# Performance work log

Measured on AMD Instinct MI355X. Metric: run time of the kernel, lower is better.

## Reference

```python
import jax, jax.numpy as jnp
import numpy as np

T = 8192        # tokens (batch*seq)
D = 1024        # d_model
H = 4096        # expert hidden = 4*d_model
E = 16          # num_expert
K = 2           # moe_top_k


def setup_inputs() -> dict:
    key = jax.random.key(0)
    ks = jax.random.split(key, 7)
    s_in = 1.0 / np.sqrt(D)
    s_h = 1.0 / np.sqrt(H)
    return {
        "moe_inp": jax.random.normal(ks[0], (T, D), dtype=jnp.float32),
        "Wg": jax.random.normal(ks[1], (D, E), dtype=jnp.float32) * s_in,
        "bg": jnp.zeros((E,), dtype=jnp.float32),
        "W1": jax.random.normal(ks[2], (E, D, H), dtype=jnp.float32) * s_in,
        "b1": jnp.zeros((E, H), dtype=jnp.float32),
        "W2": jax.random.normal(ks[3], (E, H, D), dtype=jnp.float32) * s_h,
        "b2": jnp.zeros((E, D), dtype=jnp.float32),
    }


def reference(moe_inp, Wg, bg, W1, b1, W2, b2):
    # --- NaiveGate: linear -> top-k -> softmax over selected logits ---
    logits = moe_inp @ Wg + bg                      # [T, E]
    topk_val, topk_idx = jax.lax.top_k(logits, K)   # [T, K]
    gate_score = jax.nn.softmax(topk_val, axis=-1)  # [T, K]

    # Per-(token, expert) combine weight: sum of gate scores of slots routed to e.
    # Equivalent to scatter(dispatch) -> expert MLP -> gather(combine) weighted sum.
    onehot = jax.nn.one_hot(topk_idx, E, dtype=moe_inp.dtype)  # [T, K, E]
    comb_w = jnp.einsum('tk,tke->te', gate_score, onehot)      # [T, E]

    out = jnp.zeros_like(moe_inp)
    for e in range(E):  # fixed small expert count
        h = jax.nn.relu(moe_inp @ W1[e] + b1[e])   # [T, H]
        y = h @ W2[e] + b2[e]                      # [T, D]
        out = out + comb_w[:, e:e + 1] * y
    return out
```

## Files before the change

### kernel.cpp

```cpp
#include <hip/hip_runtime.h>
#include <hip/hip_bf16.h>
#include <stdint.h>


#define Tn 8192
#define Dn 1024
#define Hn 4096
#define En 16

typedef __attribute__((ext_vector_type(8))) short bf16x8;
typedef __attribute__((ext_vector_type(4))) float f32x4;

__device__ __forceinline__ unsigned short f2bf(float f) {
    union { __hip_bfloat16 h; unsigned short u; } cv;
    cv.h = __float2bfloat16(f);
    return cv.u;
}
__device__ __forceinline__ float bf2f(unsigned short u) {
    union { unsigned int i; float f; } cv;
    cv.i = ((unsigned int)u) << 16;
    return cv.f;
}

__device__ __forceinline__ void gload_lds16(const void* gptr, void* lptr) {
    __builtin_amdgcn_global_load_lds(
        (const __attribute__((address_space(1))) uint32_t*)gptr,
        (__attribute__((address_space(3))) uint32_t*)lptr, 16, 0, 0);
}

__device__ __forceinline__ int swz_tile(int v, int total) {
    int q = total >> 3, r = total & 7;
    int x = v & 7, k = v >> 3;
    int b = (x < r) ? x * (q + 1) : r * (q + 1) + (x - r) * q;
    return b + k;
}

__device__ __forceinline__ int find_e(const int* __restrict__ mb, int gm) {
    int e = 0;
#pragma unroll
    for (int i = 1; i < En; i++) e += (mb[i] <= gm) ? 1 : 0;
    return e;
}

__device__ __forceinline__ void waitvm4()  { asm volatile("s_waitcnt vmcnt(4)" ::: "memory"); }
__device__ __forceinline__ void waitvm0()  { asm volatile("s_waitcnt vmcnt(0)" ::: "memory"); }
__device__ __forceinline__ void barrier_raw() { asm volatile("s_barrier" ::: "memory"); }

__device__ __forceinline__ bool better(float va, int ia, float vb, int ib) {
    return (va > vb) || (va == vb && ia < ib);
}

__global__ __launch_bounds__(256) void gate_kernel(
    const float* __restrict__ x, const float* __restrict__ Wg,
    const float* __restrict__ bg,
    int* cnt, int* tok_e, int* tok_pos, float* tok_w)
{
    __shared__ float wgt[16 * 1028];
    int tid = threadIdx.x;
    int t0 = blockIdx.x * 16;

#pragma unroll
    for (int i = 0; i < 64; i++) {
        int idx = i * 256 + tid;
        int k = idx >> 4, e = idx & 15;
        wgt[e * 1028 + k] = Wg[idx];
    }
    __syncthreads();

    int tok = tid >> 4, e = tid & 15;
    const float4* xr = reinterpret_cast<const float4*>(x + (size_t)(t0 + tok) * Dn);
    const float4* wr = reinterpret_cast<const float4*>(&wgt[e * 1028]);
    float acc = 0.f;
#pragma unroll 8
    for (int q = 0; q < 256; q++) {
        float4 xv = xr[q], wv = wr[q];
        acc += xv.x * wv.x + xv.y * wv.y + xv.z * wv.z + xv.w * wv.w;
    }
    acc += bg[e];

    float v0 = acc, v1 = -1e30f;
    int i0 = e, i1 = -1;
#pragma unroll
    for (int m = 1; m < 16; m <<= 1) {
        float ov0 = __shfl_xor(v0, m, 16); int oi0 = __shfl_xor(i0, m, 16);
        float ov1 = __shfl_xor(v1, m, 16); int oi1 = __shfl_xor(i1, m, 16);
        if (better(ov0, oi0, v0, i0)) {
            if (better(v0, i0, ov1, oi1)) { v1 = v0; i1 = i0; }
            else                          { v1 = ov1; i1 = oi1; }
            v0 = ov0; i0 = oi0;
        } else if (better(ov0, oi0, v1, i1)) {
            v1 = ov0; i1 = oi0;
        }
    }
    if (e == 0) {
        float ex = __expf(v1 - v0);
        float w0 = 1.f / (1.f + ex);
        float w1 = ex / (1.f + ex);
        int p0 = atomicAdd(&cnt[i0], 1);
        int p1 = atomicAdd(&cnt[i1], 1);
        int t = t0 + tok;
        tok_e[t * 2 + 0] = i0; tok_e[t * 2 + 1] = i1;
        tok_pos[t * 2 + 0] = p0; tok_pos[t * 2 + 1] = p1;
        tok_w[t * 2 + 0] = w0; tok_w[t * 2 + 1] = w1;
    }
}

__global__ void scan_kernel(const int* cnt, int* base, int* mb)
{
    if (threadIdx.x == 0 && blockIdx.x == 0) {
        int b = 0, m = 0;
        for (int e = 0; e < En; e++) {
            base[e] = b; mb[e] = m;
            b += cnt[e];
            m += (cnt[e] + 127) >> 7;
        }
        base[En] = b; mb[En] = m;
    }
}

__global__ __launch_bounds__(256) void gather_kernel(
    const float* __restrict__ x, const int* tok_e, const int* tok_pos,
    const int* base, unsigned short* xg)
{
    int t = blockIdx.x; int tid = threadIdx.x;
    int e0 = tok_e[2 * t], e1 = tok_e[2 * t + 1];
    int r0 = base[e0] + tok_pos[2 * t];
    int r1 = base[e1] + tok_pos[2 * t + 1];
    float4 v = *reinterpret_cast<const float4*>(x + (size_t)t * Dn + tid * 4);
    ushort4 u;
    u.x = f2bf(v.x); u.y = f2bf(v.y); u.z = f2bf(v.z); u.w = f2bf(v.w);
    *reinterpret_cast<ushort4*>(xg + (size_t)r0 * Dn + tid * 4) = u;
    *reinterpret_cast<ushort4*>(xg + (size_t)r1 * Dn + tid * 4) = u;
}

__global__ __launch_bounds__(512) void convT_kernel(
    const float* __restrict__ src, unsigned short* __restrict__ dst, int R, int C)
{
    int e = blockIdx.z;
    const float* s = src + (size_t)e * R * C;
    unsigned short* d = dst + (size_t)e * R * C;
    __shared__ float tile[64][65];
    int r0 = blockIdx.y * 64, c0 = blockIdx.x * 64;
    int tr = threadIdx.x >> 4;
    int tc4 = (threadIdx.x & 15) * 4;
    float4 v0 = *reinterpret_cast<const float4*>(s + (size_t)(r0 + tr) * C + c0 + tc4);
    float4 v1 = *reinterpret_cast<const float4*>(s + (size_t)(r0 + tr + 32) * C + c0 + tc4);
    tile[tr][tc4 + 0] = v0.x; tile[tr][tc4 + 1] = v0.y;
    tile[tr][tc4 + 2] = v0.z; tile[tr][tc4 + 3] = v0.w;
    tile[tr + 32][tc4 + 0] = v1.x; tile[tr + 32][tc4 + 1] = v1.y;
    tile[tr + 32][tc4 + 2] = v1.z; tile[tr + 32][tc4 + 3] = v1.w;
    __syncthreads();
    ushort4 u0, u1;
    u0.x = f2bf(tile[tc4 + 0][tr]);      u1.x = f2bf(tile[tc4 + 0][tr + 32]);
    u0.y = f2bf(tile[tc4 + 1][tr]);      u1.y = f2bf(tile[tc4 + 1][tr + 32]);
    u0.z = f2bf(tile[tc4 + 2][tr]);      u1.z = f2bf(tile[tc4 + 2][tr + 32]);
    u0.w = f2bf(tile[tc4 + 3][tr]);      u1.w = f2bf(tile[tc4 + 3][tr + 32]);
    *reinterpret_cast<ushort4*>(d + (size_t)(c0 + tr) * R + r0 + tc4) = u0;
    *reinterpret_cast<ushort4*>(d + (size_t)(c0 + tr + 32) * R + r0 + tc4) = u1;
}

template<bool G1>
__global__ __launch_bounds__(256, 3) void gemm128_kernel(
    const unsigned short* __restrict__ Ag, const unsigned short* __restrict__ Bg,
    const float* __restrict__ bias, unsigned short* __restrict__ outb,
    const int* __restrict__ cnt, const int* __restrict__ base,
    const int* __restrict__ mb)
{
    constexpr int KDIM = G1 ? Dn : Hn;
    constexpr int NOUT = G1 ? Hn : Dn;
    constexpr int NTN = NOUT / 128;
    constexpr int NT = KDIM / 32;
    __shared__ unsigned short ldsA[3][128 * 32];
    __shared__ unsigned short ldsB[3][128 * 32];

    int totalgm = mb[En];
    int total = totalgm * NTN;

    int tid = threadIdx.x;
    int lane = tid & 63;
    int w = tid >> 6;
    int wm = (w >> 1) * 64, wn = (w & 1) * 64;
    int lr16 = lane & 15, lk = lane >> 4;
    int lj = lk * 4;

    int r0t = tid >> 2;
    int r1t = (tid + 256) >> 2;
    int col0 = (tid & 3) ^ (r0t & 3);
    int col1 = (tid & 3) ^ (r1t & 3);

    int aoff[4], boff[4];
#pragma unroll
    for (int m = 0; m < 4; m++) {
        int row = wm + m * 16 + lr16;
        aoff[m] = row * 32 + ((lk ^ (row & 3)) << 3);
    }
#pragma unroll
    for (int n = 0; n < 4; n++) {
        int row = wn + n * 16 + lr16;
        boff[n] = row * 32 + ((lk ^ (row & 3)) << 3);
    }

    for (int v = blockIdx.x; v < total; v += gridDim.x) {
        int tile = swz_tile(v, total);
        int nt = tile / totalgm;
        int gm = tile - nt * totalgm;
        int e = find_e(mb, gm);
        int mtile = gm - mb[e];
        int M_e = cnt[e];
        int m0 = mtile * 128, n0 = nt * 128;
        int rowbase0 = base[e] + m0;
        const unsigned short* Ab = Ag + (size_t)rowbase0 * KDIM;
        const unsigned short* Bb = Bg + ((size_t)e * NOUT + n0) * KDIM;

        const unsigned short* aS0 = Ab + (size_t)r0t * KDIM + col0 * 8;
        const unsigned short* aS1 = Ab + (size_t)r1t * KDIM + col1 * 8;
        const unsigned short* bS0 = Bb + (size_t)r0t * KDIM + col0 * 8;
        const unsigned short* bS1 = Bb + (size_t)r1t * KDIM + col1 * 8;

        f32x4 acc[4][4];
#pragma unroll
        for (int m = 0; m < 4; m++)
#pragma unroll
            for (int n = 0; n < 4; n++) acc[m][n] = (f32x4){0.f, 0.f, 0.f, 0.f};

        auto stage = [&](int t, int sl) {
            char* sa = (char*)ldsA[sl];
            char* sb = (char*)ldsB[sl];
            int k0 = t * 32;
            gload_lds16(aS0 + k0, sa + tid * 16);
            gload_lds16(aS1 + k0, sa + (tid + 256) * 16);
            gload_lds16(bS0 + k0, sb + tid * 16);
            gload_lds16(bS1 + k0, sb + (tid + 256) * 16);
        };

        stage(0, 0);
        stage(1, 1);

        int cur = 0, nxt2 = 2;
        for (int t = 0; t < NT; ++t) {
            if (t + 1 < NT) waitvm4();
            else            waitvm0();
            barrier_raw();
            if (t + 2 < NT) stage(t + 2, nxt2);
            const unsigned short* sa = ldsA[cur];
            const unsigned short* sb = ldsB[cur];
            bf16x8 a[4], b[4];
#pragma unroll
            for (int n = 0; n < 4; n++) b[n] = *(const bf16x8*)(sb + boff[n]);
#pragma unroll
            for (int m = 0; m < 4; m++) a[m] = *(const bf16x8*)(sa + aoff[m]);
            __builtin_amdgcn_s_setprio(1);
#pragma unroll
            for (int m = 0; m < 4; m++)
#pragma unroll
                for (int n = 0; n < 4; n++)
                    acc[m][n] = __builtin_amdgcn_mfma_f32_16x16x32_bf16(b[n], a[m], acc[m][n], 0, 0, 0);
            __builtin_amdgcn_s_setprio(0);
            cur = (cur == 2) ? 0 : cur + 1;
            nxt2 = (nxt2 == 2) ? 0 : nxt2 + 1;
        }

        const float* be = bias + (size_t)e * NOUT;
#pragma unroll
        for (int m = 0; m < 4; m++) {
            int rt = wm + m * 16 + lr16;
            if (m0 + rt < M_e) {
                size_t rowoff = (size_t)(rowbase0 + rt) * NOUT;
#pragma unroll
                for (int n = 0; n < 4; n++) {
                    int col0e = n0 + wn + n * 16 + lj;
                    float4 bs = *reinterpret_cast<const float4*>(be + col0e);
                    float v0 = acc[m][n][0] + bs.x;
                    float v1 = acc[m][n][1] + bs.y;
                    float v2 = acc[m][n][2] + bs.z;
                    float v3 = acc[m][n][3] + bs.w;
                    ushort4 u;
                    if constexpr (G1) {
                        u.x = f2bf(fmaxf(v0, 0.f));
                        u.y = f2bf(fmaxf(v1, 0.f));
                        u.z = f2bf(fmaxf(v2, 0.f));
                        u.w = f2bf(fmaxf(v3, 0.f));
                    } else {
                        u.x = f2bf(v0); u.y = f2bf(v1);
                        u.z = f2bf(v2); u.w = f2bf(v3);
                    }
                    *reinterpret_cast<ushort4*>(outb + rowoff + col0e) = u;
                }
            }
        }
    }
}

__global__ __launch_bounds__(256) void combine_kernel(
    const unsigned short* __restrict__ y,
    const int* __restrict__ tok_e, const int* __restrict__ tok_pos,
    const int* __restrict__ base, const float* __restrict__ tok_w,
    float* __restrict__ out)
{
    int t = blockIdx.x, tid = threadIdx.x;
    int e0 = tok_e[2 * t], e1 = tok_e[2 * t + 1];
    int r0 = base[e0] + tok_pos[2 * t];
    int r1 = base[e1] + tok_pos[2 * t + 1];
    float w0 = tok_w[2 * t], w1 = tok_w[2 * t + 1];
    ushort4 a = *reinterpret_cast<const ushort4*>(y + (size_t)r0 * Dn + tid * 4);
    ushort4 b = *reinterpret_cast<const ushort4*>(y + (size_t)r1 * Dn + tid * 4);
    float4 o;
    o.x = w0 * bf2f(a.x) + w1 * bf2f(b.x);
    o.y = w0 * bf2f(a.y) + w1 * bf2f(b.y);
    o.z = w0 * bf2f(a.z) + w1 * bf2f(b.z);
    o.w = w0 * bf2f(a.w) + w1 * bf2f(b.w);
    *reinterpret_cast<float4*>(out + (size_t)t * Dn + tid * 4) = o;
}

extern "C" void kernel_launch(void* const* d_in, const int* in_sizes, int n_in,
                              void* d_out, int out_size, void* d_ws, size_t ws_size,
                              hipStream_t stream)
{
    const float* x  = (const float*)d_in[0];
    const float* Wg = (const float*)d_in[1];
    const float* bg = (const float*)d_in[2];
    const float* W1 = (const float*)d_in[3];
    const float* b1 = (const float*)d_in[4];
    const float* W2 = (const float*)d_in[5];
    const float* b2 = (const float*)d_in[6];
    float* out = (float*)d_out;

    char* ws = (char*)d_ws;
    size_t off = 0;
    auto alloc = [&](size_t bytes) {
        size_t o = off; off += (bytes + 255) & ~(size_t)255; return o;
    };
    const int ROWS = Tn * 2;
    const int RCAP = ROWS + 256;

    unsigned short* Wt = (unsigned short*)(ws + alloc((size_t)En * Hn * Dn * 2));
    unsigned short* xg = (unsigned short*)(ws + alloc((size_t)RCAP * Dn * 2));
    unsigned short* hg = (unsigned short*)(ws + alloc((size_t)RCAP * Hn * 2));
    unsigned short* yv = (unsigned short*)(ws + alloc((size_t)RCAP * Dn * 2));
    int*   cnt     = (int*)(ws + alloc(En * 4));
    int*   base    = (int*)(ws + alloc((En + 1) * 4));
    int*   mb      = (int*)(ws + alloc((En + 1) * 4));
    int*   tok_e   = (int*)(ws + alloc(Tn * 2 * 4));
    int*   tok_pos = (int*)(ws + alloc(Tn * 2 * 4));
    float* tok_w   = (float*)(ws + alloc(Tn * 2 * 4));
    (void)ws_size; (void)in_sizes; (void)n_in; (void)out_size;

    hipMemsetAsync(cnt, 0, En * 4, stream);

    gate_kernel<<<Tn / 16, 256, 0, stream>>>(x, Wg, bg, cnt, tok_e, tok_pos, tok_w);
    scan_kernel<<<1, 64, 0, stream>>>(cnt, base, mb);
    gather_kernel<<<Tn, 256, 0, stream>>>(x, tok_e, tok_pos, base, xg);

    convT_kernel<<<dim3(Hn / 64, Dn / 64, En), 512, 0, stream>>>(W1, Wt, Dn, Hn);
    gemm128_kernel<true><<<768, 256, 0, stream>>>(
        xg, Wt, b1, hg, cnt, base, mb);

    convT_kernel<<<dim3(Dn / 64, Hn / 64, En), 512, 0, stream>>>(W2, Wt, Hn, Dn);
    gemm128_kernel<false><<<768, 256, 0, stream>>>(
        hg, Wt, b2, yv, cnt, base, mb);

    combine_kernel<<<Tn, 256, 0, stream>>>(yv, tok_e, tok_pos, base, tok_w, out);
}
```

Baseline: 742.7 us.

## Switch expert GEMM to double-buffered LDS with 8-chunk swizzle and higher occupancy

Expert GEMM drops from triple to double buffering (48KB to 32KB of LDS per block), allowing 5 blocks per CU instead of 3, and the persistent grid grows from 768 to 1280 blocks. The LDS layout packs two 32-wide K rows into one 64-element line with an XOR swizzle over 8 chunks, aiming to reduce bank conflicts. The cost is a shallower prefetch: each iteration waits for all outstanding loads (vmcnt 0), so latency hiding has to come from more resident waves rather than a deeper pipeline. Register pressure under launch_bounds(256,5) may also force spills.

```diff
diff --git a/kernel.cpp b/kernel.cpp
--- a/kernel.cpp
+++ b/kernel.cpp
@@ -42,7 +42,6 @@
     return e;
 }
 
-__device__ __forceinline__ void waitvm4()  { asm volatile("s_waitcnt vmcnt(4)" ::: "memory"); }
 __device__ __forceinline__ void waitvm0()  { asm volatile("s_waitcnt vmcnt(0)" ::: "memory"); }
 __device__ __forceinline__ void barrier_raw() { asm volatile("s_barrier" ::: "memory"); }
 
@@ -160,7 +159,7 @@
 }
 
 template<bool G1>
-__global__ __launch_bounds__(256, 3) void gemm128_kernel(
+__global__ __launch_bounds__(256, 5) void gemm128_kernel(
     const unsigned short* __restrict__ Ag, const unsigned short* __restrict__ Bg,
     const float* __restrict__ bias, unsigned short* __restrict__ outb,
     const int* __restrict__ cnt, const int* __restrict__ base,
@@ -170,8 +169,8 @@
     constexpr int NOUT = G1 ? Hn : Dn;
     constexpr int NTN = NOUT / 128;
     constexpr int NT = KDIM / 32;
-    __shared__ unsigned short ldsA[3][128 * 32];
-    __shared__ unsigned short ldsB[3][128 * 32];
+    __shared__ unsigned short ldsA[2][64 * 64];
+    __shared__ unsigned short ldsB[2][64 * 64];
 
     int totalgm = mb[En];
     int total = totalgm * NTN;
@@ -183,21 +182,25 @@
     int lr16 = lane & 15, lk = lane >> 4;
     int lj = lk * 4;
 
-    int r0t = tid >> 2;
-    int r1t = (tid + 256) >> 2;
-    int col0 = (tid & 3) ^ (r0t & 3);
-    int col1 = (tid & 3) ^ (r1t & 3);
+    int lrow0 = tid >> 3;
+    int lrow1 = (tid + 256) >> 3;
+    int ch0 = (tid & 7) ^ (lrow0 & 7);
+    int ch1 = (tid & 7) ^ (lrow1 & 7);
+    int grow0 = lrow0 * 2 + (ch0 >> 2), kc0 = ch0 & 3;
+    int grow1 = lrow1 * 2 + (ch1 >> 2), kc1 = ch1 & 3;
 
     int aoff[4], boff[4];
 #pragma unroll
     for (int m = 0; m < 4; m++) {
         int row = wm + m * 16 + lr16;
-        aoff[m] = row * 32 + ((lk ^ (row & 3)) << 3);
+        int lr = row >> 1;
+        aoff[m] = lr * 64 + (((((row & 1) << 2) | lk) ^ (lr & 7)) << 3);
     }
 #pragma unroll
     for (int n = 0; n < 4; n++) {
         int row = wn + n * 16 + lr16;
-        boff[n] = row * 32 + ((lk ^ (row & 3)) << 3);
+        int lr = row >> 1;
+        boff[n] = lr * 64 + (((((row & 1) << 2) | lk) ^ (lr & 7)) << 3);
     }
 
     for (int v = blockIdx.x; v < total; v += gridDim.x) {
@@ -212,10 +215,10 @@
         const unsigned short* Ab = Ag + (size_t)rowbase0 * KDIM;
         const unsigned short* Bb = Bg + ((size_t)e * NOUT + n0) * KDIM;
 
-        const unsigned short* aS0 = Ab + (size_t)r0t * KDIM + col0 * 8;
-        const unsigned short* aS1 = Ab + (size_t)r1t * KDIM + col1 * 8;
-        const unsigned short* bS0 = Bb + (size_t)r0t * KDIM + col0 * 8;
-        const unsigned short* bS1 = Bb + (size_t)r1t * KDIM + col1 * 8;
+        const unsigned short* aS0 = Ab + (size_t)grow0 * KDIM + kc0 * 8;
+        const unsigned short* aS1 = Ab + (size_t)grow1 * KDIM + kc1 * 8;
+        const unsigned short* bS0 = Bb + (size_t)grow0 * KDIM + kc0 * 8;
+        const unsigned short* bS1 = Bb + (size_t)grow1 * KDIM + kc1 * 8;
 
         f32x4 acc[4][4];
 #pragma unroll
@@ -223,9 +226,9 @@
 #pragma unroll
             for (int n = 0; n < 4; n++) acc[m][n] = (f32x4){0.f, 0.f, 0.f, 0.f};
 
-        auto stage = [&](int t, int sl) {
-            char* sa = (char*)ldsA[sl];
-            char* sb = (char*)ldsB[sl];
+        auto stage = [&](int t) {
+            char* sa = (char*)ldsA[t & 1];
+            char* sb = (char*)ldsB[t & 1];
             int k0 = t * 32;
             gload_lds16(aS0 + k0, sa + tid * 16);
             gload_lds16(aS1 + k0, sa + (tid + 256) * 16);
@@ -233,17 +236,15 @@
             gload_lds16(bS1 + k0, sb + (tid + 256) * 16);
         };
 
-        stage(0, 0);
-        stage(1, 1);
-
-        int cur = 0, nxt2 = 2;
+        stage(0);
+
         for (int t = 0; t < NT; ++t) {
-            if (t + 1 < NT) waitvm4();
-            else            waitvm0();
+            waitvm0();
             barrier_raw();
-            if (t + 2 < NT) stage(t + 2, nxt2);
-            const unsigned short* sa = ldsA[cur];
-            const unsigned short* sb = ldsB[cur];
+            if (t + 1 < NT) stage(t + 1);
+            asm volatile("" ::: "memory");
+            const unsigned short* sa = ldsA[t & 1];
+            const unsigned short* sb = ldsB[t & 1];
             bf16x8 a[4], b[4];
 #pragma unroll
             for (int n = 0; n < 4; n++) b[n] = *(const bf16x8*)(sb + boff[n]);
@@ -256,8 +257,6 @@
                 for (int n = 0; n < 4; n++)
                     acc[m][n] = __builtin_amdgcn_mfma_f32_16x16x32_bf16(b[n], a[m], acc[m][n], 0, 0, 0);
             __builtin_amdgcn_s_setprio(0);
-            cur = (cur == 2) ? 0 : cur + 1;
-            nxt2 = (nxt2 == 2) ? 0 : nxt2 + 1;
         }
 
         const float* be = bias + (size_t)e * NOUT;
@@ -352,11 +351,11 @@
     gather_kernel<<<Tn, 256, 0, stream>>>(x, tok_e, tok_pos, base, xg);
 
     convT_kernel<<<dim3(Hn / 64, Dn / 64, En), 512, 0, stream>>>(W1, Wt, Dn, Hn);
-    gemm128_kernel<true><<<768, 256, 0, stream>>>(
+    gemm128_kernel<true><<<1280, 256, 0, stream>>>(
         xg, Wt, b1, hg, cnt, base, mb);
 
     convT_kernel<<<dim3(Dn / 64, Hn / 64, En), 512, 0, stream>>>(W2, Wt, Hn, Dn);
-    gemm128_kernel<false><<<768, 256, 0, stream>>>(
+    gemm128_kernel<false><<<1280, 256, 0, stream>>>(
         hg, Wt, b2, yv, cnt, base, mb);
 
     combine_kernel<<<Tn, 256, 0, stream>>>(yv, tok_e, tok_pos, base, tok_w, out);
```

New measurement: 1.669 ms. 125% more time.
